# Kernel tuning notes

Hardware: AMD Instinct MI355X
Metric: run time of the kernel (lower is better)

The kernel has to match this reference:

```python
import jax, jax.numpy as jnp
import numpy as np

EPS = 1e-8


def _laplace_normalize(edge_row, edge_col, edge_vals, num_nodes):
    # D_r^{-1/2} A D_c^{-1/2} as in laplace_transform
    deg_r = jax.ops.segment_sum(edge_vals, edge_row, num_segments=num_nodes)
    deg_c = jax.ops.segment_sum(edge_vals, edge_col, num_segments=num_nodes)
    inv_r = 1.0 / (jnp.sqrt(deg_r) + EPS)
    inv_c = 1.0 / (jnp.sqrt(deg_c) + EPS)
    return edge_vals * inv_r[edge_row] * inv_c[edge_col]


def _l2norm(x):
    # F.normalize(p=2, dim=1): x / max(||x||, eps) with eps=1e-12
    n = jnp.sqrt(jnp.sum(x * x, axis=1, keepdims=True))
    return x / jnp.maximum(n, 1e-12)


def setup_inputs() -> dict:
    key = jax.random.key(0)
    k1, k2, k3, k4, k5, k6 = jax.random.split(key, 6)
    N, D, E, B = 100000, 64, 3200000, 4096
    node_features = jax.random.normal(k1, (N, D), dtype=jnp.float32)
    edge_row = jax.random.randint(k2, (E,), 0, N, dtype=jnp.int32)
    edge_col = jax.random.randint(k3, (E,), 0, N, dtype=jnp.int32)
    edge_vals = jnp.ones((E,), dtype=jnp.float32)
    a_id = jax.random.randint(k4, (B,), 0, N, dtype=jnp.int32)
    pos_id = jax.random.randint(k5, (B,), 0, N, dtype=jnp.int32)
    neg_id = jax.random.randint(k6, (B,), 0, N, dtype=jnp.int32)
    return {"node_features": node_features, "edge_row": edge_row,
            "edge_col": edge_col, "edge_vals": edge_vals,
            "a_id": a_id, "pos_id": pos_id, "neg_id": neg_id}


def reference(node_features, edge_row, edge_col, edge_vals, a_id, pos_id, neg_id):
    num_nodes = node_features.shape[0]
    num_layers = 3
    norm_vals = _laplace_normalize(edge_row, edge_col, edge_vals, num_nodes)

    # one_propagate: repeated spmm + per-layer L2 normalize, mean over layers
    features = node_features
    acc = node_features  # layer-0 term of the running sum (not normalized)
    for _ in range(num_layers):
        msgs = norm_vals[:, None] * features[edge_col]  # [E, D]
        features = jax.ops.segment_sum(msgs, edge_row, num_segments=num_nodes)
        acc = acc + _l2norm(features)
    node_rep = acc / (num_layers + 1)

    # BPR loss over batch
    a = node_rep[a_id]
    pos_pred = jnp.sum(a * node_rep[pos_id], axis=1)
    neg_pred = jnp.sum(a * node_rep[neg_id], axis=1)
    loss = jnp.mean(-jax.nn.log_sigmoid(pos_pred - neg_pred))
    return loss
```

## Files before the change

kernel.cpp:

```cpp
#include <hip/hip_runtime.h>
#include <math.h>

#define DDIM 64
#define BUCKET 1024
#define LRSHIFT 17
#define CMASK 0x1FFFF
#define LRMASK 0x3FF
#define NBLK 512
#define TPB_BIN 512
#define TPB_CP 512
#define MAXNB 128

typedef unsigned long long ull;
typedef _Float16 half2_t __attribute__((ext_vector_type(2)));

__device__ inline unsigned int bf16_hi(float v) {
    unsigned int a = __float_as_uint(v);
    return (a + 0x7fffu + ((a >> 16) & 1u)) & 0xffff0000u;
}

__device__ inline unsigned int pk_f16x2(float lo, float hi) {
    return __builtin_bit_cast(unsigned int, __builtin_amdgcn_cvt_pkrtz(lo, hi));
}

__global__ void init_fill_kernel(int* __restrict__ gfill_r, int* __restrict__ gfill_c,
                                 int NB, int cap) {
    int k = blockIdx.x * blockDim.x + threadIdx.x;
    if (k < NB) {
        gfill_r[k * 16] = k * cap;
        gfill_c[k * 16] = k * cap;
    }
}

__global__ __launch_bounds__(TPB_BIN)
void binning_kernel(const int* __restrict__ erow, const int* __restrict__ ecol,
                    const float* __restrict__ evals,
                    int* __restrict__ gfill_r, int* __restrict__ gfill_c,
                    ull* __restrict__ br, unsigned int* __restrict__ bc,
                    int E, int NB, int chunk) {
    __shared__ int hr[8][MAXNB];
    __shared__ int hc[8][MAXNB];
    __shared__ int fr[MAXNB];
    __shared__ int fc[MAXNB];
    int t = threadIdx.x;
    int wv = t >> 6;
    for (int k = t; k < 8 * MAXNB; k += TPB_BIN) { (&hr[0][0])[k] = 0; (&hc[0][0])[k] = 0; }
    __syncthreads();
    int lo = blockIdx.x * chunk;
    int hi = min(E, lo + chunk);
    int nq = (hi - lo) >> 2;
    int rem = (hi - lo) & 3;
    for (int p = t; p < nq; p += TPB_BIN) {
        int i = lo + 4 * p;
        int4 r4 = *(const int4*)(erow + i);
        int4 c4 = *(const int4*)(ecol + i);
        atomicAdd(&hr[wv][r4.x >> 10], 1);
        atomicAdd(&hr[wv][r4.y >> 10], 1);
        atomicAdd(&hr[wv][r4.z >> 10], 1);
        atomicAdd(&hr[wv][r4.w >> 10], 1);
        atomicAdd(&hc[wv][c4.x >> 10], 1);
        atomicAdd(&hc[wv][c4.y >> 10], 1);
        atomicAdd(&hc[wv][c4.z >> 10], 1);
        atomicAdd(&hc[wv][c4.w >> 10], 1);
    }
    if (t == 0) {
        for (int i = hi - rem; i < hi; i++) {
            atomicAdd(&hr[0][erow[i] >> 10], 1);
            atomicAdd(&hc[0][ecol[i] >> 10], 1);
        }
    }
    __syncthreads();
    if (t < NB) {
        int sr = 0, sc = 0;
        #pragma unroll
        for (int w2 = 0; w2 < 8; w2++) { sr += hr[w2][t]; sc += hc[w2][t]; }
        fr[t] = atomicAdd(&gfill_r[t * 16], sr);
        fc[t] = atomicAdd(&gfill_c[t * 16], sc);
    }
    __syncthreads();
    for (int p = t; p < nq; p += TPB_BIN) {
        int i = lo + 4 * p;
        int4 r4 = *(const int4*)(erow + i);
        int4 c4 = *(const int4*)(ecol + i);
        float4 v4 = *(const float4*)(evals + i);
        int pos0 = atomicAdd(&fr[r4.x >> 10], 1);
        int pos1 = atomicAdd(&fr[r4.y >> 10], 1);
        int pos2 = atomicAdd(&fr[r4.z >> 10], 1);
        int pos3 = atomicAdd(&fr[r4.w >> 10], 1);
        br[pos0] = ((ull)__float_as_uint(v4.x) << 32) | ((ull)(r4.x & 1023) << LRSHIFT) | (unsigned)c4.x;
        br[pos1] = ((ull)__float_as_uint(v4.y) << 32) | ((ull)(r4.y & 1023) << LRSHIFT) | (unsigned)c4.y;
        br[pos2] = ((ull)__float_as_uint(v4.z) << 32) | ((ull)(r4.z & 1023) << LRSHIFT) | (unsigned)c4.z;
        br[pos3] = ((ull)__float_as_uint(v4.w) << 32) | ((ull)(r4.w & 1023) << LRSHIFT) | (unsigned)c4.w;
        int q0 = atomicAdd(&fc[c4.x >> 10], 1);
        int q1 = atomicAdd(&fc[c4.y >> 10], 1);
        int q2 = atomicAdd(&fc[c4.z >> 10], 1);
        int q3 = atomicAdd(&fc[c4.w >> 10], 1);
        bc[q0] = bf16_hi(v4.x) | (unsigned)(c4.x & 1023);
        bc[q1] = bf16_hi(v4.y) | (unsigned)(c4.y & 1023);
        bc[q2] = bf16_hi(v4.z) | (unsigned)(c4.z & 1023);
        bc[q3] = bf16_hi(v4.w) | (unsigned)(c4.w & 1023);
    }
    if (t == 0) {
        for (int i = hi - rem; i < hi; i++) {
            int r = erow[i], c = ecol[i];
            float v = evals[i];
            int pos = atomicAdd(&fr[r >> 10], 1);
            br[pos] = ((ull)__float_as_uint(v) << 32) | ((ull)(r & 1023) << LRSHIFT) | (unsigned)c;
            int pos2 = atomicAdd(&fc[c >> 10], 1);
            bc[pos2] = bf16_hi(v) | (unsigned)(c & 1023);
        }
    }
}

__global__ __launch_bounds__(TPB_CP)
void count_kernel(const ull* __restrict__ br, const unsigned int* __restrict__ bc,
                  const int* __restrict__ gfill_r, const int* __restrict__ gfill_c,
                  int* __restrict__ subcnt, float* __restrict__ subds,
                  float* __restrict__ subdsc, int cap) {
    __shared__ int cnt[BUCKET];
    __shared__ float ds[BUCKET];
    __shared__ float dsc[BUCKET];
    int b = blockIdx.x >> 3, ch = blockIdx.x & 7;
    int t = threadIdx.x;
    for (int k = t; k < BUCKET; k += TPB_CP) { cnt[k] = 0; ds[k] = 0.0f; dsc[k] = 0.0f; }
    __syncthreads();
    int s = b * cap;
    int e = gfill_r[b * 16];
    int len = ((((e - s) + 7) >> 3) + 1) & ~1;
    int cs = s + ch * len, ce = min(e, cs + len);
    int m = cs + ((ce - cs) & ~1);
    for (int i = cs + 2 * t; i < m; i += 2 * TPB_CP) {
        ull p0 = br[i];
        ull p1 = br[i + 1];
        int lr0 = (int)((p0 >> LRSHIFT) & LRMASK);
        int lr1 = (int)((p1 >> LRSHIFT) & LRMASK);
        atomicAdd(&cnt[lr0], 1);
        atomicAdd(&cnt[lr1], 1);
        atomicAdd(&ds[lr0], __uint_as_float((unsigned)(p0 >> 32)));
        atomicAdd(&ds[lr1], __uint_as_float((unsigned)(p1 >> 32)));
    }
    if (t == 0 && m < ce) {
        ull p = br[m];
        int lr = (int)((p >> LRSHIFT) & LRMASK);
        atomicAdd(&cnt[lr], 1);
        atomicAdd(&ds[lr], __uint_as_float((unsigned)(p >> 32)));
    }
    int e2 = gfill_c[b * 16];
    int len2 = ((((e2 - s) + 7) >> 3) + 1) & ~1;
    int cs2 = s + ch * len2, ce2 = min(e2, cs2 + len2);
    int m2 = cs2 + ((ce2 - cs2) & ~1);
    for (int i = cs2 + 2 * t; i < m2; i += 2 * TPB_CP) {
        uint2 p = *(const uint2*)(bc + i);
        atomicAdd(&dsc[p.x & 0x3FFu], __uint_as_float(p.x & 0xffff0000u));
        atomicAdd(&dsc[p.y & 0x3FFu], __uint_as_float(p.y & 0xffff0000u));
    }
    if (t == 0 && m2 < ce2) {
        unsigned int p = bc[m2];
        atomicAdd(&dsc[p & 0x3FFu], __uint_as_float(p & 0xffff0000u));
    }
    __syncthreads();
    size_t base = ((size_t)b * 8 + ch) * BUCKET;
    for (int k = t; k < BUCKET; k += TPB_CP) {
        subcnt[base + k] = cnt[k];
        subds[base + k]  = ds[k];
        subdsc[base + k] = dsc[k];
    }
}

__global__ __launch_bounds__(1024)
void combine_kernel(int* __restrict__ subcnt, const float* __restrict__ subds,
                    const float* __restrict__ subdsc,
                    int* __restrict__ rowstart, int* __restrict__ rowend,
                    float* __restrict__ inv_r, float* __restrict__ inv_c,
                    int N, int cap) {
    __shared__ int tot[BUCKET];
    int b = blockIdx.x, t = threadIdx.x;
    size_t base = (size_t)b * 8 * BUCKET;
    int c8[8];
    int sum = 0;
    #pragma unroll
    for (int c = 0; c < 8; c++) { c8[c] = subcnt[base + c * BUCKET + t]; sum += c8[c]; }
    int sum2 = (sum + 1) & ~1;
    tot[t] = sum2;
    __syncthreads();
    for (int off = 1; off < BUCKET; off <<= 1) {
        int v = (t >= off) ? tot[t - off] : 0;
        __syncthreads();
        tot[t] += v;
        __syncthreads();
    }
    int excl = tot[t] - sum2;
    int node = b * BUCKET + t;
    int s = b * cap;
    if (node < N) {
        rowstart[node] = s + excl;
        rowend[node]   = s + excl + sum;
    }
    int run = s + excl;
    #pragma unroll
    for (int c = 0; c < 8; c++) { int v = c8[c]; subcnt[base + c * BUCKET + t] = run; run += v; }
    float d = 0.0f, dc = 0.0f;
    #pragma unroll
    for (int c = 0; c < 8; c++) { d += subds[base + c * BUCKET + t]; dc += subdsc[base + c * BUCKET + t]; }
    inv_r[b * BUCKET + t] = 1.0f / (sqrtf(d) + 1e-8f);
    inv_c[b * BUCKET + t] = 1.0f / (sqrtf(dc) + 1e-8f);
}

__global__ __launch_bounds__(TPB_CP)
void place_kernel(const ull* __restrict__ br, const int* __restrict__ gfill_r,
                  const int* __restrict__ pbase, const float* __restrict__ inv_r,
                  const float* __restrict__ inv_c,
                  int2* __restrict__ cw, int cap) {
    __shared__ int fill[BUCKET];
    __shared__ float irs[BUCKET];
    int b = blockIdx.x >> 3, ch = blockIdx.x & 7;
    int t = threadIdx.x;
    size_t pb = ((size_t)b * 8 + ch) * BUCKET;
    for (int k = t; k < BUCKET; k += TPB_CP) {
        fill[k] = pbase[pb + k];
        irs[k]  = inv_r[b * BUCKET + k];
    }
    __syncthreads();
    int s = b * cap;
    int e = gfill_r[b * 16];
    int len = ((((e - s) + 7) >> 3) + 1) & ~1;
    int cs = s + ch * len, ce = min(e, cs + len);
    int m = cs + ((ce - cs) & ~1);
    for (int i = cs + 2 * t; i < m; i += 2 * TPB_CP) {
        ull p0 = br[i];
        ull p1 = br[i + 1];
        int c0 = (int)(p0 & CMASK), c1 = (int)(p1 & CMASK);
        int lr0 = (int)((p0 >> LRSHIFT) & LRMASK);
        int lr1 = (int)((p1 >> LRSHIFT) & LRMASK);
        float v0 = __uint_as_float((unsigned)(p0 >> 32));
        float v1 = __uint_as_float((unsigned)(p1 >> 32));
        int pos0 = atomicAdd(&fill[lr0], 1);
        int pos1 = atomicAdd(&fill[lr1], 1);
        float w0 = v0 * inv_c[c0] * irs[lr0];
        float w1 = v1 * inv_c[c1] * irs[lr1];
        int2 pk0; pk0.x = c0; pk0.y = (int)pk_f16x2(w0, w0);
        int2 pk1; pk1.x = c1; pk1.y = (int)pk_f16x2(w1, w1);
        cw[pos0] = pk0;
        cw[pos1] = pk1;
    }
    if (t == 0 && m < ce) {
        ull p = br[m];
        int c = (int)(p & CMASK);
        int lr = (int)((p >> LRSHIFT) & LRMASK);
        float v = __uint_as_float((unsigned)(p >> 32));
        int pos = atomicAdd(&fill[lr], 1);
        float wv = v * inv_c[c] * irs[lr];
        int2 pk; pk.x = c; pk.y = (int)pk_f16x2(wv, wv);
        cw[pos] = pk;
    }
}

__global__ void cvt_kernel(const float* __restrict__ src, float* __restrict__ acc,
                           unsigned int* __restrict__ dst, long n4) {
    long i = (long)blockIdx.x * blockDim.x + threadIdx.x;
    if (i < n4) {
        float4 v = ((const float4*)src)[i];
        ((float4*)acc)[i] = v;
        uint2 o;
        o.x = pk_f16x2(v.x, v.y);
        o.y = pk_f16x2(v.z, v.w);
        ((uint2*)dst)[i] = o;
    }
}

__global__ __launch_bounds__(256)
void spmm_f16_kernel(const int* __restrict__ rowstart, const int* __restrict__ rowend,
                     const int2* __restrict__ cw,
                     const unsigned short* __restrict__ fin,
                     unsigned short* __restrict__ fout,
                     float* __restrict__ acc, int N) {
    int wid = blockIdx.x * (blockDim.x >> 6) + (threadIdx.x >> 6);
    if (wid >= N) return;
    int lane = threadIdx.x & 63;
    int g = lane >> 3;
    int h = lane & 7;
    int s = rowstart[wid], e = rowend[wid];
    half2_t a2[8];
    #pragma unroll
    for (int k = 0; k < 8; k++) a2[k] = (half2_t)0;

    int nfull = (e - s) >> 4;
    int base = s;
    for (int it = 0; it < nfull; it++, base += 16) {
        int j0 = base + 2 * g;
        int4 p = *(const int4*)(cw + j0);
        uint4 q0 = ((const uint4*)(fin + ((long)p.x << 6)))[h];
        uint4 q1 = ((const uint4*)(fin + ((long)p.z << 6)))[h];
        half2_t w0 = __builtin_bit_cast(half2_t, (unsigned)p.y);
        half2_t w1 = __builtin_bit_cast(half2_t, (unsigned)p.w);
        a2[0] += w0 * __builtin_bit_cast(half2_t, q0.x);
        a2[1] += w0 * __builtin_bit_cast(half2_t, q0.y);
        a2[2] += w0 * __builtin_bit_cast(half2_t, q0.z);
        a2[3] += w0 * __builtin_bit_cast(half2_t, q0.w);
        a2[4] += w1 * __builtin_bit_cast(half2_t, q1.x);
        a2[5] += w1 * __builtin_bit_cast(half2_t, q1.y);
        a2[6] += w1 * __builtin_bit_cast(half2_t, q1.z);
        a2[7] += w1 * __builtin_bit_cast(half2_t, q1.w);
    }
    if (base < e) {
        int j0 = base + 2 * g, j1 = j0 + 1;
        int4 p = *(const int4*)(cw + j0);
        int c0 = p.x & CMASK, c1 = p.z & CMASK;
        half2_t w0 = (j0 < e) ? __builtin_bit_cast(half2_t, (unsigned)p.y) : (half2_t)0;
        half2_t w1 = (j1 < e) ? __builtin_bit_cast(half2_t, (unsigned)p.w) : (half2_t)0;
        uint4 q0 = ((const uint4*)(fin + ((long)c0 << 6)))[h];
        uint4 q1 = ((const uint4*)(fin + ((long)c1 << 6)))[h];
        a2[0] += w0 * __builtin_bit_cast(half2_t, q0.x);
        a2[1] += w0 * __builtin_bit_cast(half2_t, q0.y);
        a2[2] += w0 * __builtin_bit_cast(half2_t, q0.z);
        a2[3] += w0 * __builtin_bit_cast(half2_t, q0.w);
        a2[4] += w1 * __builtin_bit_cast(half2_t, q1.x);
        a2[5] += w1 * __builtin_bit_cast(half2_t, q1.y);
        a2[6] += w1 * __builtin_bit_cast(half2_t, q1.z);
        a2[7] += w1 * __builtin_bit_cast(half2_t, q1.w);
    }

    float a[8];
    #pragma unroll
    for (int k = 0; k < 4; k++) {
        a[2 * k]     = (float)a2[k][0] + (float)a2[k + 4][0];
        a[2 * k + 1] = (float)a2[k][1] + (float)a2[k + 4][1];
    }
    #pragma unroll
    for (int k = 0; k < 8; k++) {
        a[k] += __shfl_xor(a[k], 8);
        a[k] += __shfl_xor(a[k], 16);
        a[k] += __shfl_xor(a[k], 32);
    }
    float ss = 0.0f;
    #pragma unroll
    for (int k = 0; k < 8; k++) ss += a[k] * a[k];
    ss += __shfl_xor(ss, 1);
    ss += __shfl_xor(ss, 2);
    ss += __shfl_xor(ss, 4);
    float s2 = 1.0f / fmaxf(sqrtf(ss), 1e-12f);
    if (g == 0) {
        uint4 o;
        o.x = pk_f16x2(a[0], a[1]);
        o.y = pk_f16x2(a[2], a[3]);
        o.z = pk_f16x2(a[4], a[5]);
        o.w = pk_f16x2(a[6], a[7]);
        ((uint4*)(fout + ((long)wid << 6)))[h] = o;
        float4* ap = (float4*)(acc + ((long)wid << 6)) + (h << 1);
        float4 c0 = ap[0], c1 = ap[1];
        c0.x += a[0] * s2; c0.y += a[1] * s2; c0.z += a[2] * s2; c0.w += a[3] * s2;
        c1.x += a[4] * s2; c1.y += a[5] * s2; c1.z += a[6] * s2; c1.w += a[7] * s2;
        ap[0] = c0;
        ap[1] = c1;
    }
}

__global__ void loss_terms_kernel(const float* __restrict__ acc,
                                  const int* __restrict__ a_id, const int* __restrict__ p_id,
                                  const int* __restrict__ n_id,
                                  float* __restrict__ terms, int B) {
    long gid = (long)blockIdx.x * blockDim.x + threadIdx.x;
    int b = (int)(gid >> 6);
    int lane = threadIdx.x & 63;
    if (b < B) {
        int ia = a_id[b], ip = p_id[b], in2 = n_id[b];
        float a = acc[(long)ia * DDIM + lane];
        float p = acc[(long)ip * DDIM + lane];
        float n = acc[(long)in2 * DDIM + lane];
        float dp = a * p, dn = a * n;
        #pragma unroll
        for (int off = 1; off < 64; off <<= 1) { dp += __shfl_xor(dp, off); dn += __shfl_xor(dn, off); }
        if (lane == 0) {
            float x = (dp - dn) * 0.0625f;
            terms[b] = fmaxf(-x, 0.0f) + log1pf(expf(-fabsf(x)));
        }
    }
}

__global__ void reduce_kernel(const float* __restrict__ terms, float* __restrict__ out, int B) {
    __shared__ float sm[256];
    float s = 0.0f;
    for (int i = threadIdx.x; i < B; i += 256) s += terms[i];
    sm[threadIdx.x] = s;
    __syncthreads();
    for (int stride = 128; stride > 0; stride >>= 1) {
        if (threadIdx.x < stride) sm[threadIdx.x] += sm[threadIdx.x + stride];
        __syncthreads();
    }
    if (threadIdx.x == 0) out[0] = sm[0] / (float)B;
}

extern "C" void kernel_launch(void* const* d_in, const int* in_sizes, int n_in,
                              void* d_out, int out_size, void* d_ws, size_t ws_size,
                              hipStream_t stream) {
    const float* nf    = (const float*)d_in[0];
    const int*   erow  = (const int*)d_in[1];
    const int*   ecol  = (const int*)d_in[2];
    const float* evals = (const float*)d_in[3];
    const int*   a_id  = (const int*)d_in[4];
    const int*   p_id  = (const int*)d_in[5];
    const int*   n_id  = (const int*)d_in[6];

    int N = in_sizes[0] / DDIM;
    int E = in_sizes[1];
    int B = in_sizes[4];
    int NB = (N + BUCKET - 1) / BUCKET;
    int chunk = (((E + NBLK - 1) / NBLK) + 3) & ~3;
    int Npad = NB * BUCKET;

    long capl = ((long)E * BUCKET) / N;
    int cap = (int)(capl + capl / 12 + 2048);
    cap = (cap + 63) & ~63;

    size_t regionBytes = (size_t)cap * NB * 8;
    size_t featB32 = (size_t)N * DDIM * 4;
    size_t featB16 = (size_t)N * DDIM * 2;
    size_t subBytes = (size_t)NB * 8 * BUCKET * 4;

    char* w = (char*)d_ws;
    ull*  br     = (ull*)w;
    char* regAp  = w;                 w += regionBytes;
    unsigned int* bc = (unsigned int*)w;
    int2* cw     = (int2*)w;          w += regionBytes;
    float* acc   = (float*)w;         w += featB32;
    int* subcnt  = (int*)w;           w += subBytes;
    float* subds = (float*)w;         w += subBytes;
    float* subdsc= (float*)w;         w += subBytes;
    float* inv_c = (float*)w;         w += (size_t)Npad * 4;
    float* inv_r = (float*)w;         w += (size_t)Npad * 4;
    int* rowstart= (int*)w;           w += (size_t)N * 4;
    int* rowend  = (int*)w;           w += (size_t)N * 4;
    int* gfill_r = (int*)w;           w += (size_t)NB * 16 * 4;
    int* gfill_c = (int*)w;           w += (size_t)NB * 16 * 4;
    float* terms = (float*)w;         w += (size_t)B * 4;

    unsigned short* fb0 = (unsigned short*)regAp;
    unsigned short* fb1 = (unsigned short*)(regAp + featB16);

    init_fill_kernel<<<1, 128, 0, stream>>>(gfill_r, gfill_c, NB, cap);
    binning_kernel<<<NBLK, TPB_BIN, 0, stream>>>(erow, ecol, evals, gfill_r, gfill_c,
                                                 br, bc, E, NB, chunk);
    count_kernel<<<NB * 8, TPB_CP, 0, stream>>>(br, bc, gfill_r, gfill_c,
                                                subcnt, subds, subdsc, cap);
    combine_kernel<<<NB, 1024, 0, stream>>>(subcnt, subds, subdsc, rowstart, rowend,
                                            inv_r, inv_c, N, cap);
    place_kernel<<<NB * 8, TPB_CP, 0, stream>>>(br, gfill_r, subcnt, inv_r, inv_c, cw, cap);

    long n4 = (long)N * DDIM / 4;
    cvt_kernel<<<(unsigned)((n4 + 255) / 256), 256, 0, stream>>>(nf, acc, (unsigned int*)fb0, n4);

    unsigned spmmGrid = (unsigned)((N + 3) / 4);
    spmm_f16_kernel<<<spmmGrid, 256, 0, stream>>>(rowstart, rowend, cw, fb0, fb1, acc, N);
    spmm_f16_kernel<<<spmmGrid, 256, 0, stream>>>(rowstart, rowend, cw, fb1, fb0, acc, N);
    spmm_f16_kernel<<<spmmGrid, 256, 0, stream>>>(rowstart, rowend, cw, fb0, fb1, acc, N);

    loss_terms_kernel<<<(unsigned)(((long)B * 64 + 255) / 256), 256, 0, stream>>>(
        acc, a_id, p_id, n_id, terms, B);
    reduce_kernel<<<1, 256, 0, stream>>>(terms, (float*)d_out, B);
}
```

Baseline: 436.4 us.

## Pack edge col and fp16 weight into 32 bits, keep accumulator in fp16

Edge entries now pack a 17-bit column index with a truncated fp16 weight into one 32-bit word, halving the edge-stream traffic in each SpMM pass and in placement. The layer accumulator moves from fp32 to fp16, which halves its read-modify-write traffic and the cvt kernel's writes. The last SpMM layer also skips writing its unused feature output. In exchange the weights lose their lowest mantissa bit, the accumulator loses precision, and column indices must fit in 17 bits.

```diff
diff --git a/kernel.cpp b/kernel.cpp
--- a/kernel.cpp
+++ b/kernel.cpp
@@ -21,6 +21,10 @@
 
 __device__ inline unsigned int pk_f16x2(float lo, float hi) {
     return __builtin_bit_cast(unsigned int, __builtin_amdgcn_cvt_pkrtz(lo, hi));
+}
+
+__device__ inline half2_t dup_lo16(unsigned int s) {
+    return __builtin_bit_cast(half2_t, __builtin_amdgcn_perm(0u, s, 0x01000100u));
 }
 
 __global__ void init_fill_kernel(int* __restrict__ gfill_r, int* __restrict__ gfill_c,
@@ -210,7 +214,7 @@
 void place_kernel(const ull* __restrict__ br, const int* __restrict__ gfill_r,
                   const int* __restrict__ pbase, const float* __restrict__ inv_r,
                   const float* __restrict__ inv_c,
-                  int2* __restrict__ cw, int cap) {
+                  unsigned int* __restrict__ cw, int cap) {
     __shared__ int fill[BUCKET];
     __shared__ float irs[BUCKET];
     int b = blockIdx.x >> 3, ch = blockIdx.x & 7;
@@ -238,10 +242,8 @@
         int pos1 = atomicAdd(&fill[lr1], 1);
         float w0 = v0 * inv_c[c0] * irs[lr0];
         float w1 = v1 * inv_c[c1] * irs[lr1];
-        int2 pk0; pk0.x = c0; pk0.y = (int)pk_f16x2(w0, w0);
-        int2 pk1; pk1.x = c1; pk1.y = (int)pk_f16x2(w1, w1);
-        cw[pos0] = pk0;
-        cw[pos1] = pk1;
+        cw[pos0] = ((unsigned)c0 << 15) | ((pk_f16x2(w0, w0) & 0xFFFFu) >> 1);
+        cw[pos1] = ((unsigned)c1 << 15) | ((pk_f16x2(w1, w1) & 0xFFFFu) >> 1);
     }
     if (t == 0 && m < ce) {
         ull p = br[m];
@@ -250,30 +252,29 @@
         float v = __uint_as_float((unsigned)(p >> 32));
         int pos = atomicAdd(&fill[lr], 1);
         float wv = v * inv_c[c] * irs[lr];
-        int2 pk; pk.x = c; pk.y = (int)pk_f16x2(wv, wv);
-        cw[pos] = pk;
-    }
-}
-
-__global__ void cvt_kernel(const float* __restrict__ src, float* __restrict__ acc,
+        cw[pos] = ((unsigned)c << 15) | ((pk_f16x2(wv, wv) & 0xFFFFu) >> 1);
+    }
+}
+
+__global__ void cvt_kernel(const float* __restrict__ src, unsigned int* __restrict__ acc16,
                            unsigned int* __restrict__ dst, long n4) {
     long i = (long)blockIdx.x * blockDim.x + threadIdx.x;
     if (i < n4) {
         float4 v = ((const float4*)src)[i];
-        ((float4*)acc)[i] = v;
         uint2 o;
         o.x = pk_f16x2(v.x, v.y);
         o.y = pk_f16x2(v.z, v.w);
+        ((uint2*)acc16)[i] = o;
         ((uint2*)dst)[i] = o;
     }
 }
 
 __global__ __launch_bounds__(256)
 void spmm_f16_kernel(const int* __restrict__ rowstart, const int* __restrict__ rowend,
-                     const int2* __restrict__ cw,
+                     const unsigned int* __restrict__ cw,
                      const unsigned short* __restrict__ fin,
                      unsigned short* __restrict__ fout,
-                     float* __restrict__ acc, int N) {
+                     unsigned short* __restrict__ acc16, int N, int writeOut) {
     int wid = blockIdx.x * (blockDim.x >> 6) + (threadIdx.x >> 6);
     if (wid >= N) return;
     int lane = threadIdx.x & 63;
@@ -288,11 +289,13 @@
     int base = s;
     for (int it = 0; it < nfull; it++, base += 16) {
         int j0 = base + 2 * g;
-        int4 p = *(const int4*)(cw + j0);
-        uint4 q0 = ((const uint4*)(fin + ((long)p.x << 6)))[h];
-        uint4 q1 = ((const uint4*)(fin + ((long)p.z << 6)))[h];
-        half2_t w0 = __builtin_bit_cast(half2_t, (unsigned)p.y);
-        half2_t w1 = __builtin_bit_cast(half2_t, (unsigned)p.w);
+        uint2 pw = *(const uint2*)(cw + j0);
+        int c0 = (int)(pw.x >> 15);
+        int c1 = (int)(pw.y >> 15);
+        uint4 q0 = ((const uint4*)(fin + ((long)c0 << 6)))[h];
+        uint4 q1 = ((const uint4*)(fin + ((long)c1 << 6)))[h];
+        half2_t w0 = dup_lo16(pw.x << 1);
+        half2_t w1 = dup_lo16(pw.y << 1);
         a2[0] += w0 * __builtin_bit_cast(half2_t, q0.x);
         a2[1] += w0 * __builtin_bit_cast(half2_t, q0.y);
         a2[2] += w0 * __builtin_bit_cast(half2_t, q0.z);
@@ -304,10 +307,11 @@
     }
     if (base < e) {
         int j0 = base + 2 * g, j1 = j0 + 1;
-        int4 p = *(const int4*)(cw + j0);
-        int c0 = p.x & CMASK, c1 = p.z & CMASK;
-        half2_t w0 = (j0 < e) ? __builtin_bit_cast(half2_t, (unsigned)p.y) : (half2_t)0;
-        half2_t w1 = (j1 < e) ? __builtin_bit_cast(half2_t, (unsigned)p.w) : (half2_t)0;
+        uint2 pw = *(const uint2*)(cw + j0);
+        int c0 = (int)(pw.x >> 15);
+        int c1 = (int)(pw.y >> 15);
+        half2_t w0 = (j0 < e) ? dup_lo16(pw.x << 1) : (half2_t)0;
+        half2_t w1 = (j1 < e) ? dup_lo16(pw.y << 1) : (half2_t)0;
         uint4 q0 = ((const uint4*)(fin + ((long)c0 << 6)))[h];
         uint4 q1 = ((const uint4*)(fin + ((long)c1 << 6)))[h];
         a2[0] += w0 * __builtin_bit_cast(half2_t, q0.x);
@@ -345,17 +349,24 @@
         o.y = pk_f16x2(a[2], a[3]);
         o.z = pk_f16x2(a[4], a[5]);
         o.w = pk_f16x2(a[6], a[7]);
-        ((uint4*)(fout + ((long)wid << 6)))[h] = o;
-        float4* ap = (float4*)(acc + ((long)wid << 6)) + (h << 1);
-        float4 c0 = ap[0], c1 = ap[1];
-        c0.x += a[0] * s2; c0.y += a[1] * s2; c0.z += a[2] * s2; c0.w += a[3] * s2;
-        c1.x += a[4] * s2; c1.y += a[5] * s2; c1.z += a[6] * s2; c1.w += a[7] * s2;
-        ap[0] = c0;
-        ap[1] = c1;
-    }
-}
-
-__global__ void loss_terms_kernel(const float* __restrict__ acc,
+        if (writeOut) ((uint4*)(fout + ((long)wid << 6)))[h] = o;
+        uint4* ap = (uint4*)(acc16 + ((long)wid << 6)) + h;
+        uint4 old = *ap;
+        uint4 inc;
+        inc.x = pk_f16x2(a[0] * s2, a[1] * s2);
+        inc.y = pk_f16x2(a[2] * s2, a[3] * s2);
+        inc.z = pk_f16x2(a[4] * s2, a[5] * s2);
+        inc.w = pk_f16x2(a[6] * s2, a[7] * s2);
+        uint4 nw;
+        nw.x = __builtin_bit_cast(unsigned int, __builtin_bit_cast(half2_t, old.x) + __builtin_bit_cast(half2_t, inc.x));
+        nw.y = __builtin_bit_cast(unsigned int, __builtin_bit_cast(half2_t, old.y) + __builtin_bit_cast(half2_t, inc.y));
+        nw.z = __builtin_bit_cast(unsigned int, __builtin_bit_cast(half2_t, old.z) + __builtin_bit_cast(half2_t, inc.z));
+        nw.w = __builtin_bit_cast(unsigned int, __builtin_bit_cast(half2_t, old.w) + __builtin_bit_cast(half2_t, inc.w));
+        *ap = nw;
+    }
+}
+
+__global__ void loss_terms_kernel(const unsigned short* __restrict__ acc16,
                                   const int* __restrict__ a_id, const int* __restrict__ p_id,
                                   const int* __restrict__ n_id,
                                   float* __restrict__ terms, int B) {
@@ -364,9 +375,9 @@
     int lane = threadIdx.x & 63;
     if (b < B) {
         int ia = a_id[b], ip = p_id[b], in2 = n_id[b];
-        float a = acc[(long)ia * DDIM + lane];
-        float p = acc[(long)ip * DDIM + lane];
-        float n = acc[(long)in2 * DDIM + lane];
+        float a = (float)__builtin_bit_cast(_Float16, acc16[(long)ia * DDIM + lane]);
+        float p = (float)__builtin_bit_cast(_Float16, acc16[(long)ip * DDIM + lane]);
+        float n = (float)__builtin_bit_cast(_Float16, acc16[(long)in2 * DDIM + lane]);
         float dp = a * p, dn = a * n;
         #pragma unroll
         for (int off = 1; off < 64; off <<= 1) { dp += __shfl_xor(dp, off); dn += __shfl_xor(dn, off); }
@@ -412,17 +423,17 @@
     int cap = (int)(capl + capl / 12 + 2048);
     cap = (cap + 63) & ~63;
 
-    size_t regionBytes = (size_t)cap * NB * 8;
-    size_t featB32 = (size_t)N * DDIM * 4;
+    size_t regionA = (size_t)cap * NB * 8;
+    size_t regionB = (size_t)cap * NB * 4;
     size_t featB16 = (size_t)N * DDIM * 2;
     size_t subBytes = (size_t)NB * 8 * BUCKET * 4;
 
     char* w = (char*)d_ws;
     ull*  br     = (ull*)w;
-    char* regAp  = w;                 w += regionBytes;
+    char* regAp  = w;                 w += regionA;
     unsigned int* bc = (unsigned int*)w;
-    int2* cw     = (int2*)w;          w += regionBytes;
-    float* acc   = (float*)w;         w += featB32;
+    unsigned int* cw = (unsigned int*)w;  w += regionB + 64;
+    unsigned int* acc16 = (unsigned int*)w;  w += featB16;
     int* subcnt  = (int*)w;           w += subBytes;
     float* subds = (float*)w;         w += subBytes;
     float* subdsc= (float*)w;         w += subBytes;
@@ -447,14 +458,17 @@
     place_kernel<<<NB * 8, TPB_CP, 0, stream>>>(br, gfill_r, subcnt, inv_r, inv_c, cw, cap);
 
     long n4 = (long)N * DDIM / 4;
-    cvt_kernel<<<(unsigned)((n4 + 255) / 256), 256, 0, stream>>>(nf, acc, (unsigned int*)fb0, n4);
+    cvt_kernel<<<(unsigned)((n4 + 255) / 256), 256, 0, stream>>>(nf, acc16, (unsigned int*)fb0, n4);
 
     unsigned spmmGrid = (unsigned)((N + 3) / 4);
-    spmm_f16_kernel<<<spmmGrid, 256, 0, stream>>>(rowstart, rowend, cw, fb0, fb1, acc, N);
-    spmm_f16_kernel<<<spmmGrid, 256, 0, stream>>>(rowstart, rowend, cw, fb1, fb0, acc, N);
-    spmm_f16_kernel<<<spmmGrid, 256, 0, stream>>>(rowstart, rowend, cw, fb0, fb1, acc, N);
+    spmm_f16_kernel<<<spmmGrid, 256, 0, stream>>>(rowstart, rowend, cw, fb0, fb1,
+                                                  (unsigned short*)acc16, N, 1);
+    spmm_f16_kernel<<<spmmGrid, 256, 0, stream>>>(rowstart, rowend, cw, fb1, fb0,
+                                                  (unsigned short*)acc16, N, 1);
+    spmm_f16_kernel<<<spmmGrid, 256, 0, stream>>>(rowstart, rowend, cw, fb0, fb1,
+                                                  (unsigned short*)acc16, N, 0);
 
     loss_terms_kernel<<<(unsigned)(((long)B * 64 + 255) / 256), 256, 0, stream>>>(
-        acc, a_id, p_id, n_id, terms, B);
+        (const unsigned short*)acc16, a_id, p_id, n_id, terms, B);
     reduce_kernel<<<1, 256, 0, stream>>>(terms, (float*)d_out, B);
 }
```

New measurement: 425.1 us. 2.6% less time.
